# Kernel tuning notes

Hardware: AMD Instinct MI355X
Metric: run time of the kernel (lower is better)

## Reference

```python
import jax, jax.numpy as jnp
import numpy as np

N, E, F_IN, H, OUT = 50000, 1600000, 128, 128, 32
NEG_SLOPE = 0.2


def setup_inputs() -> dict:
    key = jax.random.key(0)
    ks = jax.random.split(key, 9)
    s = lambda fan: 1.0 / np.sqrt(fan)
    x = jax.random.normal(ks[0], (N, F_IN), jnp.float32)
    edge_index = jax.random.randint(ks[1], (2, E), 0, N, jnp.int64)
    Wl1 = jax.random.normal(ks[2], (F_IN, H), jnp.float32) * s(F_IN)
    Wr1 = jax.random.normal(ks[3], (F_IN, H), jnp.float32) * s(F_IN)
    att1 = jax.random.normal(ks[4], (H,), jnp.float32) * s(H)
    b1 = jnp.zeros((H,), jnp.float32)
    Wl2 = jax.random.normal(ks[5], (H, OUT), jnp.float32) * s(H)
    Wr2 = jax.random.normal(ks[6], (H, OUT), jnp.float32) * s(H)
    att2 = jax.random.normal(ks[7], (OUT,), jnp.float32) * s(OUT)
    b2 = jnp.zeros((OUT,), jnp.float32)
    return {"x": x, "edge_index": edge_index, "Wl1": Wl1, "Wr1": Wr1,
            "att1": att1, "b1": b1, "Wl2": Wl2, "Wr2": Wr2, "att2": att2, "b2": b2}


def gatv2_layer(x, Wl, Wr, att, bias, src, dst, num_nodes):
    # PyG GATv2Conv (heads=1, concat=True, add_self_loops handled by caller)
    xl = x @ Wl  # source-side transform  [N, C]
    xr = x @ Wr  # target-side transform  [N, C]
    e = jax.nn.leaky_relu(xl[src] + xr[dst], NEG_SLOPE)  # [E, C]
    logits = e @ att  # [E]
    # segment softmax over incoming edges of each destination node
    m = jax.ops.segment_max(logits, dst, num_segments=num_nodes)  # [N]
    expv = jnp.exp(logits - m[dst])
    denom = jax.ops.segment_sum(expv, dst, num_segments=num_nodes)  # [N]
    alpha = expv / (denom[dst] + 1e-16)  # [E]
    out = jax.ops.segment_sum(xl[src] * alpha[:, None], dst, num_segments=num_nodes)
    return out + bias


def reference(x, edge_index, Wl1, Wr1, att1, b1, Wl2, Wr2, att2, b2):
    # add self-loops (PyG add_self_loops=True default)
    loops = jnp.arange(N, dtype=edge_index.dtype)
    src = jnp.concatenate([edge_index[0], loops])
    dst = jnp.concatenate([edge_index[1], loops])
    h = gatv2_layer(x, Wl1, Wr1, att1, b1, src, dst, N)
    h = jax.nn.relu(h)
    h = gatv2_layer(h, Wl2, Wr2, att2, b2, src, dst, N)
    return jax.nn.relu(h)
```

## Files before the change

### kernel.cpp

```cpp
#include <hip/hip_runtime.h>
#include <hip/hip_bf16.h>

#define N_NODES 50000
#define E_EDGES 1600000
#define E_TOT   (E_EDGES + N_NODES)
#define NEG_SLOPE 0.2f

#define NB       196
#define S1_TILE  4096
#define NT       ((E_TOT + S1_TILE - 1) / S1_TILE)
#define S2_CAP   10240
#define GB1      ((N_NODES + 127) / 128)

typedef _Float16 h2 __attribute__((ext_vector_type(2)));
typedef _Float16 h4 __attribute__((ext_vector_type(4)));
typedef _Float16 h8 __attribute__((ext_vector_type(8)));

__device__ __forceinline__ float fdot2h(h2 a, h2 b, float c)
{
#if __has_builtin(__builtin_amdgcn_fdot2)
    return __builtin_amdgcn_fdot2(a, b, c, false);
#else
    return c + (float)a[0] * (float)b[0] + (float)a[1] * (float)b[1];
#endif
}

__device__ __forceinline__ h2 habs2(h2 e)
{
    unsigned int u = __builtin_bit_cast(unsigned int, e) & 0x7FFF7FFFu;
    return __builtin_bit_cast(h2, u);
}

__device__ __forceinline__ int wave_iscan(int v, int lane)
{
#pragma unroll
    for (int off = 1; off < 64; off <<= 1) {
        int u = __shfl_up(v, off);
        if (lane >= off) v += u;
    }
    return v;
}

__global__ __launch_bounds__(256) void fused_t1_hist(
    const float* __restrict__ x,
    const float* __restrict__ Wl, const float* __restrict__ Wr,
    _Float16* __restrict__ xl, _Float16* __restrict__ xr,
    const int* __restrict__ src, const int* __restrict__ dst,
    int* __restrict__ counts, int* __restrict__ done)
{
    __shared__ h2 xs2[16][128];
    __shared__ h2 ws2[16][128];
    __shared__ int hh[NB];
    const int t = threadIdx.x;

    if (blockIdx.x >= 2 * GB1) {
        const int tile = blockIdx.x - 2 * GB1;
        if (tile == 0 && t == 0) *done = 0;
        const int base = tile * S1_TILE;
        for (int i = t; i < NB; i += 256) hh[i] = 0;
        __syncthreads();
#pragma unroll
        for (int k = 0; k < S1_TILE / 256; ++k) {
            const int i = base + k * 256 + t;
            if (i < E_TOT) {
                const int d = (i < E_EDGES) ? dst[i] : (i - E_EDGES);
                atomicAdd(&hh[d >> 8], 1);
            }
        }
        __syncthreads();
        for (int b = t; b < NB; b += 256)
            counts[tile * NB + b] = hh[b];
        return;
    }

    const int n0 = (blockIdx.x >> 1) * 128;
    const float* __restrict__ W = (blockIdx.x & 1) ? Wr : Wl;
    _Float16* __restrict__ Y = (blockIdx.x & 1) ? xr : xl;
    const int tc = t & 15;
    const int tn = t >> 4;

    float acc[2][4][2][4];
#pragma unroll
    for (int nh = 0; nh < 2; ++nh)
#pragma unroll
        for (int i = 0; i < 4; ++i)
#pragma unroll
            for (int ch = 0; ch < 2; ++ch)
#pragma unroll
                for (int j = 0; j < 4; ++j) acc[nh][i][ch][j] = 0.f;

    for (int k0 = 0; k0 < 128; k0 += 32) {
        {
            const int node = t >> 1;
            const int kh = (t & 1) * 16;
            const int gn = n0 + node;
#pragma unroll
            for (int q = 0; q < 4; ++q) {
                float4 v = make_float4(0.f, 0.f, 0.f, 0.f);
                if (gn < N_NODES)
                    v = *(const float4*)&x[(size_t)gn * 128 + k0 + kh + q * 4];
                h2 p0 = {(_Float16)v.x, (_Float16)v.y};
                h2 p1 = {(_Float16)v.z, (_Float16)v.w};
                xs2[kh / 2 + q * 2 + 0][node] = p0;
                xs2[kh / 2 + q * 2 + 1][node] = p1;
            }
        }
        {
            const int c = t & 127;
            const int kq = (t >> 7) * 16;
#pragma unroll
            for (int ii = 0; ii < 8; ++ii) {
                h2 pw = {(_Float16)W[(size_t)(k0 + kq + 2 * ii) * 128 + c],
                         (_Float16)W[(size_t)(k0 + kq + 2 * ii + 1) * 128 + c]};
                ws2[kq / 2 + ii][c] = pw;
            }
        }
        __syncthreads();
#pragma unroll 4
        for (int k2 = 0; k2 < 16; ++k2) {
            h2 a0[4], a1[4], b0[4], b1[4];
#pragma unroll
            for (int j = 0; j < 4; ++j) {
                a0[j] = xs2[k2][tn * 4 + j];
                a1[j] = xs2[k2][64 + tn * 4 + j];
                b0[j] = ws2[k2][tc * 4 + j];
                b1[j] = ws2[k2][64 + tc * 4 + j];
            }
#pragma unroll
            for (int i = 0; i < 4; ++i)
#pragma unroll
                for (int j = 0; j < 4; ++j) {
                    acc[0][i][0][j] = fdot2h(a0[i], b0[j], acc[0][i][0][j]);
                    acc[0][i][1][j] = fdot2h(a0[i], b1[j], acc[0][i][1][j]);
                    acc[1][i][0][j] = fdot2h(a1[i], b0[j], acc[1][i][0][j]);
                    acc[1][i][1][j] = fdot2h(a1[i], b1[j], acc[1][i][1][j]);
                }
        }
        __syncthreads();
    }
#pragma unroll
    for (int nh = 0; nh < 2; ++nh)
#pragma unroll
        for (int i = 0; i < 4; ++i) {
            const int node = n0 + nh * 64 + tn * 4 + i;
            if (node < N_NODES) {
#pragma unroll
                for (int ch = 0; ch < 2; ++ch) {
                    h4 v;
                    v[0] = (_Float16)acc[nh][i][ch][0];
                    v[1] = (_Float16)acc[nh][i][ch][1];
                    v[2] = (_Float16)acc[nh][i][ch][2];
                    v[3] = (_Float16)acc[nh][i][ch][3];
                    *(h4*)&Y[(size_t)node * 128 + ch * 64 + tc * 4] = v;
                }
            }
        }
}

__global__ __launch_bounds__(256) void transform2_gemm(
    const _Float16* __restrict__ h,
    const float* __restrict__ Wl, const float* __restrict__ Wr,
    _Float16* __restrict__ hl, _Float16* __restrict__ hr)
{
    __shared__ h2 xs2[16][128];
    __shared__ h2 ws2[16][64];
    const int n0 = blockIdx.x * 128;
    const int t = threadIdx.x;
    const int tc = t & 15;
    const int tn = t >> 4;

    float acc[2][4][4];
#pragma unroll
    for (int nh = 0; nh < 2; ++nh)
#pragma unroll
        for (int i = 0; i < 4; ++i)
#pragma unroll
            for (int j = 0; j < 4; ++j) acc[nh][i][j] = 0.f;

    for (int k0 = 0; k0 < 128; k0 += 32) {
        {
            const int node = t >> 1;
            const int kh = (t & 1) * 16;
            const int gn = n0 + node;
            h8 v0 = {}, v1 = {};
            if (gn < N_NODES) {
                v0 = *(const h8*)&h[(size_t)gn * 128 + k0 + kh];
                v1 = *(const h8*)&h[(size_t)gn * 128 + k0 + kh + 8];
            }
#pragma unroll
            for (int q = 0; q < 4; ++q) {
                h2 p0 = {v0[2 * q], v0[2 * q + 1]};
                h2 p1 = {v1[2 * q], v1[2 * q + 1]};
                xs2[kh / 2 + q][node] = p0;
                xs2[kh / 2 + 4 + q][node] = p1;
            }
        }
        {
            const int c = t & 63;
            const int kq = (t >> 6) * 8;
            const float* __restrict__ Wm = (c < 32) ? Wl : Wr;
            const int wc = c & 31;
#pragma unroll
            for (int ii = 0; ii < 4; ++ii) {
                h2 pw = {(_Float16)Wm[(size_t)(k0 + kq + 2 * ii) * 32 + wc],
                         (_Float16)Wm[(size_t)(k0 + kq + 2 * ii + 1) * 32 + wc]};
                ws2[kq / 2 + ii][c] = pw;
            }
        }
        __syncthreads();
#pragma unroll 4
        for (int k2 = 0; k2 < 16; ++k2) {
            h2 a0[4], a1[4], b[4];
#pragma unroll
            for (int j = 0; j < 4; ++j) {
                a0[j] = xs2[k2][tn * 4 + j];
                a1[j] = xs2[k2][64 + tn * 4 + j];
                b[j] = ws2[k2][tc * 4 + j];
            }
#pragma unroll
            for (int i = 0; i < 4; ++i)
#pragma unroll
                for (int j = 0; j < 4; ++j) {
                    acc[0][i][j] = fdot2h(a0[i], b[j], acc[0][i][j]);
                    acc[1][i][j] = fdot2h(a1[i], b[j], acc[1][i][j]);
                }
        }
        __syncthreads();
    }
    _Float16* __restrict__ Y = (tc < 8) ? hl : hr;
    const int col = (tc < 8) ? tc * 4 : tc * 4 - 32;
#pragma unroll
    for (int nh = 0; nh < 2; ++nh)
#pragma unroll
        for (int i = 0; i < 4; ++i) {
            const int node = n0 + nh * 64 + tn * 4 + i;
            if (node < N_NODES) {
                h4 v;
                v[0] = (_Float16)acc[nh][i][0];
                v[1] = (_Float16)acc[nh][i][1];
                v[2] = (_Float16)acc[nh][i][2];
                v[3] = (_Float16)acc[nh][i][3];
                *(h4*)&Y[(size_t)node * 32 + col] = v;
            }
        }
}

__global__ __launch_bounds__(512) void row_scan_base(
    const int* __restrict__ counts, int* __restrict__ rstart,
    int* __restrict__ bcount, int* __restrict__ bbase, int* __restrict__ done)
{
    __shared__ int wsum[8];
    __shared__ int amLast;
    const int b = blockIdx.x;
    const int t = threadIdx.x;
    const int lane = t & 63, wid = t >> 6;
    const int v = (t < NT) ? counts[t * NB + b] : 0;
    int inc = wave_iscan(v, lane);
    if (lane == 63) wsum[wid] = inc;
    __syncthreads();
    if (t == 0) {
        int s = 0;
#pragma unroll
        for (int w = 0; w < 8; ++w) { int u = wsum[w]; wsum[w] = s; s += u; }
    }
    __syncthreads();
    const int excl = inc - v + wsum[wid];
    if (t < NT) rstart[b * NT + t] = excl;
    if (t == 511) {
        bcount[b] = excl;
        __threadfence();
        const int old = atomicAdd(done, 1);
        amLast = (old == NB - 1) ? 1 : 0;
    }
    __syncthreads();
    if (amLast) {
        __threadfence();
        const int v2 = (t < NB) ? bcount[t] : 0;
        int inc2 = wave_iscan(v2, lane);
        if (lane == 63 && wid < 4) wsum[wid] = inc2;
        __syncthreads();
        if (t == 0) {
            int s = 0;
#pragma unroll
            for (int w = 0; w < 4; ++w) { int u = wsum[w]; wsum[w] = s; s += u; }
        }
        __syncthreads();
        if (t < 256) {
            const int excl2 = inc2 - v2 + wsum[wid];
            if (t < NB) bbase[t] = excl2;
            if (t == NB - 1) bbase[NB] = excl2 + v2;
        }
    }
}

__global__ __launch_bounds__(512) void tile_scatter(
    const int* __restrict__ src, const int* __restrict__ dst,
    const int* __restrict__ rstart, const int* __restrict__ bbase,
    unsigned int* __restrict__ bucket_data)
{
    __shared__ int hh[256];
    __shared__ int cur[NB];
    __shared__ int rs[NB];
    __shared__ int wsum[8];
    __shared__ unsigned int srt[S1_TILE];
    const int t = threadIdx.x;
    const int tile = blockIdx.x;
    const int base = tile * S1_TILE;
    const int tcount = min(S1_TILE, E_TOT - base);

    for (int i = t; i < 256; i += 512) hh[i] = 0;
    __syncthreads();

    int eb[S1_TILE / 512];
    unsigned int ee[S1_TILE / 512];
#pragma unroll
    for (int k = 0; k < S1_TILE / 512; ++k) {
        const int i = base + k * 512 + t;
        eb[k] = -1;
        if (i < E_TOT) {
            int s, d;
            if (i < E_EDGES) { s = src[i]; d = dst[i]; }
            else { s = i - E_EDGES; d = s; }
            const int b = d >> 8;
            eb[k] = b;
            ee[k] = ((unsigned)b << 24) | ((unsigned)(d & 255) << 16) | (unsigned)s;
            atomicAdd(&hh[b], 1);
        }
    }
    __syncthreads();
    {
        const int lane = t & 63, wid = t >> 6;
        const int v = (t < 256) ? hh[t] : 0;
        int inc = wave_iscan(v, lane);
        if (lane == 63 && wid < 4) wsum[wid] = inc;
        __syncthreads();
        if (t == 0) {
            int s = 0;
#pragma unroll
            for (int w = 0; w < 4; ++w) { int u = wsum[w]; wsum[w] = s; s += u; }
        }
        __syncthreads();
        if (t < NB) {
            const int excl = inc - v + wsum[wid];
            cur[t] = excl;
            rs[t] = bbase[t] + rstart[t * NT + tile] - excl;
        }
    }
    __syncthreads();
#pragma unroll
    for (int k = 0; k < S1_TILE / 512; ++k) {
        if (eb[k] >= 0) {
            const int pos = atomicAdd(&cur[eb[k]], 1);
            srt[pos] = ee[k];
        }
    }
    __syncthreads();
    for (int i = t; i < tcount; i += 512) {
        const unsigned int e = srt[i];
        bucket_data[rs[e >> 24] + i] = e;
    }
}

__global__ __launch_bounds__(1024) void bucket_sort(
    const unsigned int* __restrict__ bucket_data,
    const int* __restrict__ bbase,
    int* __restrict__ offs, unsigned short* __restrict__ sorted_src)
{
    __shared__ int hist[256];
    __shared__ int hsrc[256];
    __shared__ int cur[256];
    __shared__ int csrc[256];
    __shared__ int wsum[4];
    __shared__ unsigned int srt4[S2_CAP];
    const int b = blockIdx.x;
    const int t = threadIdx.x;
    const int lo = bbase[b], hi = bbase[b + 1];
    const int c = hi - lo;
    if (t < 256) { hist[t] = 0; hsrc[t] = 0; }
    __syncthreads();
    for (int i = t; i < c; i += 1024) {
        const unsigned int e = bucket_data[lo + i];
        atomicAdd(&hist[(e >> 16) & 255u], 1);
        atomicAdd(&hsrc[(e >> 8) & 255u], 1);
    }
    __syncthreads();
    {
        const int lane = t & 63, wid = t >> 6;
        const int v = (t < 256) ? hsrc[t] : 0;
        int inc = wave_iscan(v, lane);
        if (lane == 63 && wid < 4) wsum[wid] = inc;
        __syncthreads();
        if (t == 0) {
            int s = 0;
#pragma unroll
            for (int w = 0; w < 4; ++w) { int u = wsum[w]; wsum[w] = s; s += u; }
        }
        __syncthreads();
        if (t < 256) csrc[t] = inc - v + wsum[wid];
        __syncthreads();
    }
    {
        const int lane = t & 63, wid = t >> 6;
        const int v = (t < 256) ? hist[t] : 0;
        int inc = wave_iscan(v, lane);
        if (lane == 63 && wid < 4) wsum[wid] = inc;
        __syncthreads();
        if (t == 0) {
            int s = 0;
#pragma unroll
            for (int w = 0; w < 4; ++w) { int u = wsum[w]; wsum[w] = s; s += u; }
        }
        __syncthreads();
        if (t < 256) {
            const int excl = inc - v + wsum[wid];
            cur[t] = excl;
            const int node = b * 256 + t;
            if (node < N_NODES) offs[node] = lo + excl;
        }
    }
    if (b == 0 && t == 0) offs[N_NODES] = E_TOT;
    __syncthreads();
    for (int i = t; i < c; i += 1024) {
        const unsigned int e = bucket_data[lo + i];
        const int pos = atomicAdd(&csrc[(e >> 8) & 255u], 1);
        srt4[pos] = e;
    }
    __syncthreads();
    for (int i = t; i < c; i += 1024) {
        const unsigned int e = srt4[i];
        const int pos = atomicAdd(&cur[(e >> 16) & 255u], 1);
        sorted_src[lo + pos] = (unsigned short)(e & 0xFFFFu);
    }
}

template <int C, int LPG, typename OUT_T>
__global__ __launch_bounds__(256) void gat_edge_pass(
    const _Float16* __restrict__ xl, const _Float16* __restrict__ xr,
    const float* __restrict__ att, const float* __restrict__ bias,
    const int* __restrict__ offs, const unsigned short* __restrict__ ssrc,
    OUT_T* __restrict__ out)
{
    constexpr int GPB = 256 / LPG;
    static_assert(C == LPG * 8, "8 halves per lane");
    const int node = blockIdx.x * GPB + threadIdx.x / LPG;
    if (node >= N_NODES) return;
    const int lane = threadIdx.x % LPG;
    const int cb = lane * 8;

    h2 a6[4], a4[4], r2[4];
    {
        const h8 rv = *(const h8*)(xr + (size_t)node * C + cb);
#pragma unroll
        for (int i = 0; i < 4; ++i) {
            const float av0 = att[cb + 2 * i], av1 = att[cb + 2 * i + 1];
            h2 t6 = {(_Float16)(0.6f * av0), (_Float16)(0.6f * av1)};
            h2 t4 = {(_Float16)(0.4f * av0), (_Float16)(0.4f * av1)};
            a6[i] = t6; a4[i] = t4;
            h2 rr = {rv[2 * i], rv[2 * i + 1]};
            r2[i] = rr;
        }
    }
    float acc[8];
#pragma unroll
    for (int v = 0; v < 8; ++v) acc[v] = 0.f;
    float m = -3.0e38f, denom = 0.f;

    const int p1 = offs[node + 1];
    int p = offs[node];

    for (; p + 4 <= p1; p += 4) {
        const int s0 = ssrc[p], s1 = ssrc[p + 1];
        const int s2 = ssrc[p + 2], s3 = ssrc[p + 3];
        const h8 x0 = *(const h8*)(xl + (size_t)s0 * C + cb);
        const h8 x1 = *(const h8*)(xl + (size_t)s1 * C + cb);
        const h8 x2 = *(const h8*)(xl + (size_t)s2 * C + cb);
        const h8 x3 = *(const h8*)(xl + (size_t)s3 * C + cb);
        float d0 = 0.f, d1 = 0.f, d2 = 0.f, d3 = 0.f;
#pragma unroll
        for (int i = 0; i < 4; ++i) {
            h2 xa = {x0[2 * i], x0[2 * i + 1]};
            h2 xb = {x1[2 * i], x1[2 * i + 1]};
            h2 xc = {x2[2 * i], x2[2 * i + 1]};
            h2 xd = {x3[2 * i], x3[2 * i + 1]};
            h2 e0 = xa + r2[i], e1 = xb + r2[i];
            h2 e2 = xc + r2[i], e3 = xd + r2[i];
            d0 = fdot2h(a6[i], e0, fdot2h(a4[i], habs2(e0), d0));
            d1 = fdot2h(a6[i], e1, fdot2h(a4[i], habs2(e1), d1));
            d2 = fdot2h(a6[i], e2, fdot2h(a4[i], habs2(e2), d2));
            d3 = fdot2h(a6[i], e3, fdot2h(a4[i], habs2(e3), d3));
        }
#pragma unroll
        for (int off = LPG >> 1; off; off >>= 1) {
            d0 += __shfl_xor(d0, off);
            d1 += __shfl_xor(d1, off);
            d2 += __shfl_xor(d2, off);
            d3 += __shfl_xor(d3, off);
        }
        const float pm = fmaxf(fmaxf(d0, d1), fmaxf(d2, d3));
        if (__builtin_expect(pm > m + 8.f, 0)) {
            const float sc = __expf(m - pm);
            m = pm;
            denom *= sc;
#pragma unroll
            for (int v = 0; v < 8; ++v) acc[v] *= sc;
        }
        const float w0 = __expf(d0 - m), w1 = __expf(d1 - m);
        const float w2 = __expf(d2 - m), w3 = __expf(d3 - m);
        denom += (w0 + w1) + (w2 + w3);
        const h2 wA = {(_Float16)w0, (_Float16)w1};
        const h2 wB = {(_Float16)w2, (_Float16)w3};
#pragma unroll
        for (int v = 0; v < 8; ++v) {
            h2 pA = {x0[v], x1[v]};
            h2 pB = {x2[v], x3[v]};
            acc[v] = fdot2h(wA, pA, fdot2h(wB, pB, acc[v]));
        }
    }
    for (; p + 2 <= p1; p += 2) {
        const int s0 = ssrc[p], s1 = ssrc[p + 1];
        const h8 x0 = *(const h8*)(xl + (size_t)s0 * C + cb);
        const h8 x1 = *(const h8*)(xl + (size_t)s1 * C + cb);
        float d0 = 0.f, d1 = 0.f;
#pragma unroll
        for (int i = 0; i < 4; ++i) {
            h2 xa = {x0[2 * i], x0[2 * i + 1]};
            h2 xb = {x1[2 * i], x1[2 * i + 1]};
            h2 e0 = xa + r2[i], e1 = xb + r2[i];
            d0 = fdot2h(a6[i], e0, fdot2h(a4[i], habs2(e0), d0));
            d1 = fdot2h(a6[i], e1, fdot2h(a4[i], habs2(e1), d1));
        }
#pragma unroll
        for (int off = LPG >> 1; off; off >>= 1) {
            d0 += __shfl_xor(d0, off);
            d1 += __shfl_xor(d1, off);
        }
        const float pm = fmaxf(d0, d1);
        if (__builtin_expect(pm > m + 8.f, 0)) {
            const float sc = __expf(m - pm);
            m = pm;
            denom *= sc;
#pragma unroll
            for (int v = 0; v < 8; ++v) acc[v] *= sc;
        }
        const float w0 = __expf(d0 - m), w1 = __expf(d1 - m);
        denom += w0 + w1;
        const h2 wA = {(_Float16)w0, (_Float16)w1};
#pragma unroll
        for (int v = 0; v < 8; ++v) {
            h2 pA = {x0[v], x1[v]};
            acc[v] = fdot2h(wA, pA, acc[v]);
        }
    }
    if (p < p1) {
        const int s0 = ssrc[p];
        const h8 x0 = *(const h8*)(xl + (size_t)s0 * C + cb);
        float d0 = 0.f;
#pragma unroll
        for (int i = 0; i < 4; ++i) {
            h2 xa = {x0[2 * i], x0[2 * i + 1]};
            h2 e0 = xa + r2[i];
            d0 = fdot2h(a6[i], e0, fdot2h(a4[i], habs2(e0), d0));
        }
#pragma unroll
        for (int off = LPG >> 1; off; off >>= 1) d0 += __shfl_xor(d0, off);
        if (d0 > m + 8.f) {
            const float sc = __expf(m - d0);
            m = d0;
            denom *= sc;
#pragma unroll
            for (int v = 0; v < 8; ++v) acc[v] *= sc;
        }
        const float w0 = __expf(d0 - m);
        denom += w0;
        const h2 wA = {(_Float16)w0, (_Float16)0.f};
#pragma unroll
        for (int v = 0; v < 8; ++v) {
            h2 pA = {x0[v], x0[v]};
            acc[v] = fdot2h(wA, pA, acc[v]);
        }
    }

    const float inv = 1.f / (denom + 1e-16f);
    if constexpr (sizeof(OUT_T) == 2) {
        h8 o;
#pragma unroll
        for (int v = 0; v < 8; ++v)
            o[v] = (_Float16)fmaxf(fmaf(acc[v], inv, bias[cb + v]), 0.f);
        *(h8*)&out[(size_t)node * C + cb] = o;
    } else {
        float4 o0, o1;
        o0.x = fmaxf(fmaf(acc[0], inv, bias[cb + 0]), 0.f);
        o0.y = fmaxf(fmaf(acc[1], inv, bias[cb + 1]), 0.f);
        o0.z = fmaxf(fmaf(acc[2], inv, bias[cb + 2]), 0.f);
        o0.w = fmaxf(fmaf(acc[3], inv, bias[cb + 3]), 0.f);
        o1.x = fmaxf(fmaf(acc[4], inv, bias[cb + 4]), 0.f);
        o1.y = fmaxf(fmaf(acc[5], inv, bias[cb + 5]), 0.f);
        o1.z = fmaxf(fmaf(acc[6], inv, bias[cb + 6]), 0.f);
        o1.w = fmaxf(fmaf(acc[7], inv, bias[cb + 7]), 0.f);
        *(float4*)&out[(size_t)node * C + cb] = o0;
        *(float4*)&out[(size_t)node * C + cb + 4] = o1;
    }
}

extern "C" void kernel_launch(void* const* d_in, const int* in_sizes, int n_in,
                              void* d_out, int out_size, void* d_ws, size_t ws_size,
                              hipStream_t stream)
{
    const float* x    = (const float*)d_in[0];
    const int*   ei   = (const int*)d_in[1];
    const float* Wl1  = (const float*)d_in[2];
    const float* Wr1  = (const float*)d_in[3];
    const float* att1 = (const float*)d_in[4];
    const float* b1   = (const float*)d_in[5];
    const float* Wl2  = (const float*)d_in[6];
    const float* Wr2  = (const float*)d_in[7];
    const float* att2 = (const float*)d_in[8];
    const float* b2   = (const float*)d_in[9];
    float* out = (float*)d_out;

    const int* e_src = ei;
    const int* e_dst = ei + E_EDGES;

    char* ws = (char*)d_ws;
    _Float16* xl = (_Float16*)(ws + 0);
    _Float16* xr = (_Float16*)(ws + 25600000);
    _Float16* h  = (_Float16*)(ws + 51200000);
    unsigned short* sorted_src = (unsigned short*)(ws + 76800000);
    int* offs   = (int*)(ws + 83400192);
    int* bbase  = (int*)(ws + 83600384);
    int* bcount = (int*)(ws + 83602432);
    int* done   = (int*)(ws + 83703808);
    unsigned int* bucket_data = (unsigned int*)(ws + 51200000);
    int* counts = (int*)(ws + 58000000);
    int* rstart = (int*)(ws + 58400000);
    _Float16* hl = xl;
    _Float16* hr = xr;

    fused_t1_hist<<<2 * GB1 + NT, 256, 0, stream>>>(
        x, Wl1, Wr1, xl, xr, e_src, e_dst, counts, done);

    row_scan_base<<<NB, 512, 0, stream>>>(counts, rstart, bcount, bbase, done);

    tile_scatter<<<NT, 512, 0, stream>>>(e_src, e_dst, rstart, bbase, bucket_data);

    bucket_sort<<<NB, 1024, 0, stream>>>(bucket_data, bbase, offs, sorted_src);

    gat_edge_pass<128, 16, _Float16><<<N_NODES * 16 / 256, 256, 0, stream>>>(
        xl, xr, att1, b1, offs, sorted_src, h);

    transform2_gemm<<<(N_NODES + 127) / 128, 256, 0, stream>>>(
        h, Wl2, Wr2, hl, hr);

    gat_edge_pass<32, 4, float><<<(N_NODES * 4 + 255) / 256, 256, 0, stream>>>(
        hl, hr, att2, b2, offs, sorted_src, out);
}
```

Measured before the change: 173.2 us.

## Split each node's edge list across two lane groups and stage sorted output in LDS

The GAT edge pass now gives each destination node two lane groups. Each group processes half of the incoming edges with its own online softmax, and the two partial states (max, denominator, accumulators) are merged with cross-lane shuffles before one half writes the output. This doubles the parallelism and memory-level parallelism per node, aimed at the latency-bound gather of source features, at the cost of twice the threads and an extra merge step. Separately, bucket_sort stages the final source indices in shared memory so the global write becomes contiguous instead of scattered.

Result: faster. 165.3 us (-4.6%).

```diff
diff --git a/kernel.cpp b/kernel.cpp
--- a/kernel.cpp
+++ b/kernel.cpp
@@ -372,6 +372,7 @@
     __shared__ int csrc[256];
     __shared__ int wsum[4];
     __shared__ unsigned int srt4[S2_CAP];
+    __shared__ unsigned short srt2[S2_CAP];
     const int b = blockIdx.x;
     const int t = threadIdx.x;
     const int lo = bbase[b], hi = bbase[b + 1];
@@ -429,8 +430,11 @@
     for (int i = t; i < c; i += 1024) {
         const unsigned int e = srt4[i];
         const int pos = atomicAdd(&cur[(e >> 16) & 255u], 1);
-        sorted_src[lo + pos] = (unsigned short)(e & 0xFFFFu);
-    }
+        srt2[pos] = (unsigned short)(e & 0xFFFFu);
+    }
+    __syncthreads();
+    for (int i = t; i < c; i += 1024)
+        sorted_src[lo + i] = srt2[i];
 }
 
 template <int C, int LPG, typename OUT_T>
@@ -440,10 +444,11 @@
     const int* __restrict__ offs, const unsigned short* __restrict__ ssrc,
     OUT_T* __restrict__ out)
 {
-    constexpr int GPB = 256 / LPG;
-    static_assert(C == LPG * 8, "8 halves per lane");
-    const int node = blockIdx.x * GPB + threadIdx.x / LPG;
+    constexpr int GPN = 2 * LPG;
+    static_assert(C == LPG * 8, "8 halves per lane per half-group");
+    const int node = (blockIdx.x * 256 + threadIdx.x) / GPN;
     if (node >= N_NODES) return;
+    const int half = (threadIdx.x / LPG) & 1;
     const int lane = threadIdx.x % LPG;
     const int cb = lane * 8;
 
@@ -465,8 +470,11 @@
     for (int v = 0; v < 8; ++v) acc[v] = 0.f;
     float m = -3.0e38f, denom = 0.f;
 
-    const int p1 = offs[node + 1];
-    int p = offs[node];
+    const int p0 = offs[node];
+    const int pE = offs[node + 1];
+    const int hlen = (pE - p0 + 1) >> 1;
+    int p = half ? (p0 + hlen) : p0;
+    const int p1 = half ? pE : (p0 + hlen);
 
     for (; p + 4 <= p1; p += 4) {
         const int s0 = ssrc[p], s1 = ssrc[p + 1];
@@ -579,6 +587,21 @@
             acc[v] = fdot2h(wA, pA, acc[v]);
         }
     }
+
+    {
+        const float mo = __shfl_xor(m, LPG);
+        const float nm = fmaxf(m, mo);
+        const float sc = __expf(m - nm);
+        denom *= sc;
+        denom += __shfl_xor(denom, LPG);
+#pragma unroll
+        for (int v = 0; v < 8; ++v) {
+            acc[v] *= sc;
+            acc[v] += __shfl_xor(acc[v], LPG);
+        }
+        m = nm;
+    }
+    if (half) return;
 
     const float inv = 1.f / (denom + 1e-16f);
     if constexpr (sizeof(OUT_T) == 2) {
@@ -645,12 +668,12 @@
 
     bucket_sort<<<NB, 1024, 0, stream>>>(bucket_data, bbase, offs, sorted_src);
 
-    gat_edge_pass<128, 16, _Float16><<<N_NODES * 16 / 256, 256, 0, stream>>>(
+    gat_edge_pass<128, 16, _Float16><<<(N_NODES * 32 + 255) / 256, 256, 0, stream>>>(
         xl, xr, att1, b1, offs, sorted_src, h);
 
     transform2_gemm<<<(N_NODES + 127) / 128, 256, 0, stream>>>(
         h, Wl2, Wr2, hl, hr);
 
-    gat_edge_pass<32, 4, float><<<(N_NODES * 4 + 255) / 256, 256, 0, stream>>>(
+    gat_edge_pass<32, 4, float><<<(N_NODES * 8 + 255) / 256, 256, 0, stream>>>(
         hl, hr, att2, b2, offs, sorted_src, out);
 }
```
